# Kernel tuning notes

Measured on AMD Instinct MI355X. Metric: run time of the kernel, lower is better.

The kernel has to match this reference:

```python
import jax, jax.numpy as jnp
import numpy as np

T_LEN, E_LEN, BATCH, DIM = 32, 256, 16, 512  # topic_len, exp_len, batch, input=hidden size
HID = 512


def setup_inputs() -> dict:
    key = jax.random.key(0)
    k1, k2, k3, k4, k5, k6 = jax.random.split(key, 6)
    topic = jax.random.normal(k1, (T_LEN, BATCH, DIM), dtype=jnp.float32)
    exp_output = jax.random.normal(k2, (E_LEN, BATCH, DIM), dtype=jnp.float32)
    seq_mask = jax.random.bernoulli(k3, 0.1, (E_LEN, BATCH))  # True = masked exp position
    # nn.Linear(hidden+input, hidden): weight [HID, HID+DIM], bias [HID]
    lim1 = 1.0 / np.sqrt(HID + DIM)
    W_attn = jax.random.uniform(k4, (HID, HID + DIM), minval=-lim1, maxval=lim1, dtype=jnp.float32)
    b_attn = jax.random.uniform(k5, (HID,), minval=-lim1, maxval=lim1, dtype=jnp.float32)
    # nn.Linear(hidden, 1): weight [1, HID], bias [1]
    lim2 = 1.0 / np.sqrt(HID)
    kv, kb = jax.random.split(k6)
    v_score = jax.random.uniform(kv, (1, HID), minval=-lim2, maxval=lim2, dtype=jnp.float32)
    b_score = jax.random.uniform(kb, (1,), minval=-lim2, maxval=lim2, dtype=jnp.float32)
    return {"topic": topic, "exp_output": exp_output, "seq_mask": seq_mask,
            "W_attn": W_attn, "b_attn": b_attn, "v_score": v_score, "b_score": b_score}


def reference(topic, exp_output, seq_mask, W_attn, b_attn, v_score, b_score):
    # topic: [T, B, D]; exp_output: [E, B, D]; seq_mask: [E, B] bool
    D = topic.shape[2]
    # Split the concat-Linear: cat(topic, exp) @ W.T == topic @ W[:, :D].T + exp @ W[:, D:].T
    proj_t = jnp.einsum('tbd,hd->bth', topic, W_attn[:, :D])        # [B, T, H]
    proj_e = jnp.einsum('ebd,hd->beh', exp_output, W_attn[:, D:])   # [B, E, H]
    feat = jnp.tanh(proj_t[:, :, None, :] + proj_e[:, None, :, :] + b_attn)  # [B, T, E, H]
    energies = jnp.einsum('bteh,h->bte', feat, v_score[0]) + b_score[0]      # [B, T, E]
    # mask exp positions (broadcast over topic dim), as masked_fill(-1e12)
    energies = jnp.where(seq_mask.T[:, None, :], jnp.float32(-1e12), energies)
    attn_s1 = jax.nn.softmax(jnp.swapaxes(energies, 1, 2), axis=2)  # [B, E, T], softmax over topics
    attn_s2 = jax.nn.softmax(energies, axis=2)                      # [B, T, E], softmax over exp
    new_exp = jnp.einsum('bet,btd->bed', attn_s1, jnp.swapaxes(topic, 0, 1))       # [B, E, D]
    new_topic = jnp.einsum('bte,bed->btd', attn_s2, jnp.swapaxes(exp_output, 0, 1))  # [B, T, D]
    return new_topic, new_exp
```

## Files before the change

### kernel.cpp

```cpp
#include <hip/hip_runtime.h>
#include <hip/hip_bf16.h>
#include <cstddef>
#include <cstdint>

#define T_LEN 32
#define E_LEN 256
#define BATCH 16
#define DIM 512
#define HID 512
#define WROW 1024

#define TWO_LOG2E 2.8853900817779268f
#define LOG2E 1.4426950408889634f

typedef __attribute__((ext_vector_type(8))) short bf16x8;
typedef __attribute__((ext_vector_type(4))) float f32x4;

__device__ inline bf16x8 cvt8(float4 a, float4 b) {
    union { bf16x8 v; __hip_bfloat16 h[8]; } u;
    u.h[0] = __float2bfloat16(a.x); u.h[1] = __float2bfloat16(a.y);
    u.h[2] = __float2bfloat16(a.z); u.h[3] = __float2bfloat16(a.w);
    u.h[4] = __float2bfloat16(b.x); u.h[5] = __float2bfloat16(b.y);
    u.h[6] = __float2bfloat16(b.z); u.h[7] = __float2bfloat16(b.w);
    return u.v;
}

#define GPAD 8
#define GLDR (64 + GPAD)

__global__ __launch_bounds__(256) void gemm_fused(
    const float* __restrict__ topic, const float* __restrict__ expo,
    const float* __restrict__ W, const float* __restrict__ battn,
    float* __restrict__ EPT, float* __restrict__ EPE) {
    __shared__ __hip_bfloat16 As[64 * GLDR];
    __shared__ __hip_bfloat16 Bs[64 * GLDR];
    const int tid = threadIdx.x;
    const int by = blockIdx.y;
    const float* A; const float* Wp; const float* bias; float* C; int m0;
    if (by < 8) { A = topic; Wp = W;       bias = battn;   C = EPT; m0 = by * 64; }
    else        { A = expo;  Wp = W + DIM; bias = nullptr; C = EPE; m0 = (by - 8) * 64; }
    const int n0 = blockIdx.x * 64;
    const int w = tid >> 6;
    const int lane = tid & 63;
    const int l15 = lane & 15;
    const int g = lane >> 4;
    const int srow = tid >> 2;
    const int sc = tid & 3;

    f32x4 acc[4];
    const f32x4 z = {0.f, 0.f, 0.f, 0.f};
#pragma unroll
    for (int nt = 0; nt < 4; ++nt) acc[nt] = z;

    const float* ga = A + (size_t)(m0 + srow) * 512 + sc * 8;
    const float* gb = Wp + (size_t)(n0 + srow) * WROW + sc * 8;

    float4 a0 = *(const float4*)(ga);
    float4 a1 = *(const float4*)(ga + 4);
    float4 a2 = *(const float4*)(ga + 32);
    float4 a3 = *(const float4*)(ga + 36);
    float4 b0 = *(const float4*)(gb);
    float4 b1 = *(const float4*)(gb + 4);
    float4 b2 = *(const float4*)(gb + 32);
    float4 b3 = *(const float4*)(gb + 36);

    for (int kk = 0; kk < 8; ++kk) {
        bf16x8 av0 = cvt8(a0, a1), av1 = cvt8(a2, a3);
        bf16x8 bv0 = cvt8(b0, b1), bv1 = cvt8(b2, b3);
        if (kk < 7) {
            ga += 64; gb += 64;
            a0 = *(const float4*)(ga);
            a1 = *(const float4*)(ga + 4);
            a2 = *(const float4*)(ga + 32);
            a3 = *(const float4*)(ga + 36);
            b0 = *(const float4*)(gb);
            b1 = *(const float4*)(gb + 4);
            b2 = *(const float4*)(gb + 32);
            b3 = *(const float4*)(gb + 36);
        }
        __syncthreads();
        *(bf16x8*)&As[srow * GLDR + sc * 8] = av0;
        *(bf16x8*)&As[srow * GLDR + sc * 8 + 32] = av1;
        *(bf16x8*)&Bs[srow * GLDR + sc * 8] = bv0;
        *(bf16x8*)&Bs[srow * GLDR + sc * 8 + 32] = bv1;
        __syncthreads();
#pragma unroll
        for (int s = 0; s < 2; ++s) {
            bf16x8 af = *(const bf16x8*)&As[(w * 16 + l15) * GLDR + (s * 4 + g) * 8];
#pragma unroll
            for (int nt = 0; nt < 4; ++nt) {
                bf16x8 bf = *(const bf16x8*)&Bs[(nt * 16 + l15) * GLDR + (s * 4 + g) * 8];
                acc[nt] = __builtin_amdgcn_mfma_f32_16x16x32_bf16(af, bf, acc[nt], 0, 0, 0);
            }
        }
    }
#pragma unroll
    for (int nt = 0; nt < 4; ++nt) {
        int n = n0 + nt * 16 + l15;
        float bv = bias ? bias[n] : 0.f;
#pragma unroll
        for (int r = 0; r < 4; ++r) {
            int m = m0 + w * 16 + g * 4 + r;
            C[(size_t)m * 512 + n] = __builtin_amdgcn_exp2f((acc[nt][r] + bv) * TWO_LOG2E);
        }
    }
}

__global__ __launch_bounds__(256) void energies_k(const float* __restrict__ EPT,
                                                  const float* __restrict__ EPE,
                                                  const float* __restrict__ v,
                                                  const int* __restrict__ mask,
                                                  float* __restrict__ P) {
    const int b = blockIdx.x;
    const int tg = blockIdx.y;
    const int ech = blockIdx.z;
    const int lane = threadIdx.x & 63;
    const int w = threadIdx.x >> 6;
    const int h0 = lane * 8;
    const int e0 = ech * 16 + w * 4;

    int mk[4];
#pragma unroll
    for (int ei = 0; ei < 4; ++ei) mk[ei] = mask[(e0 + ei) * BATCH + b];

    float sv[8], spt[8][8];
    {
        float4 v0 = *(const float4*)(v + h0);
        float4 v1 = *(const float4*)(v + h0 + 4);
        sv[0] = -2.f * v0.x; sv[1] = -2.f * v0.y; sv[2] = -2.f * v0.z; sv[3] = -2.f * v0.w;
        sv[4] = -2.f * v1.x; sv[5] = -2.f * v1.y; sv[6] = -2.f * v1.z; sv[7] = -2.f * v1.w;
#pragma unroll
        for (int i = 0; i < 8; ++i) {
            const float* p = EPT + ((size_t)((tg * 8 + i) * BATCH + b)) * HID + h0;
            float4 p0 = *(const float4*)(p);
            float4 p1 = *(const float4*)(p + 4);
            spt[i][0] = p0.x; spt[i][1] = p0.y; spt[i][2] = p0.z; spt[i][3] = p0.w;
            spt[i][4] = p1.x; spt[i][5] = p1.y; spt[i][6] = p1.z; spt[i][7] = p1.w;
        }
    }
#pragma unroll
    for (int ei = 0; ei < 4; ++ei) {
        const int e = e0 + ei;
        if (mk[ei] != 0) {
            if (lane < 8)
                P[((size_t)b * T_LEN + tg * 8 + lane) * E_LEN + e] = 1e-30f;
            continue;
        }
        const float* pe = EPE + ((size_t)(e * BATCH + b)) * HID + h0;
        float4 p0 = *(const float4*)(pe);
        float4 p1 = *(const float4*)(pe + 4);
        float pr[8] = {p0.x, p0.y, p0.z, p0.w, p1.x, p1.y, p1.z, p1.w};
        float a[8] = {0.f, 0.f, 0.f, 0.f, 0.f, 0.f, 0.f, 0.f};
#pragma unroll
        for (int i = 0; i < 8; ++i) {
#pragma unroll
            for (int j = 0; j < 8; ++j) {
                float q = fmaf(spt[i][j], pr[j], 1.0f);
                float r = __builtin_amdgcn_rcpf(q);
                a[i] = fmaf(sv[j], r, a[i]);
            }
        }
#pragma unroll
        for (int i = 0; i < 8; ++i) {
            a[i] += __shfl_xor(a[i], 1);
            a[i] += __shfl_xor(a[i], 2);
            a[i] += __shfl_xor(a[i], 4);
            a[i] += __shfl_xor(a[i], 8);
        }
        const int sel = lane & 3;
        float uA = sel == 0 ? a[0] : sel == 1 ? a[1] : sel == 2 ? a[2] : a[3];
        float uB = sel == 0 ? a[4] : sel == 1 ? a[5] : sel == 2 ? a[6] : a[7];
        uA += __shfl_xor(uA, 16); uA += __shfl_xor(uA, 32);
        uB += __shfl_xor(uB, 16); uB += __shfl_xor(uB, 32);
        float u = (lane & 4) ? uB : uA;
        if (lane < 8)
            P[((size_t)b * T_LEN + tg * 8 + lane) * E_LEN + e] =
                __builtin_amdgcn_exp2f(u * LOG2E);
    }
}

__global__ __launch_bounds__(256) void epilogue_k(const float* __restrict__ P,
                                                  const float* __restrict__ topic,
                                                  const float* __restrict__ expo,
                                                  float* __restrict__ out) {
    __shared__ float smem[2560];
    const int tid = threadIdx.x;
    const int lane = tid & 63;
    const int w = tid >> 6;
    if (blockIdx.x < 512) {
        const int b = blockIdx.x >> 5;
        const int ech = (blockIdx.x >> 1) & 15;
        const int hf = blockIdx.x & 1;
        const int e0 = ech * 16 + w * 4;
        float wv[4];
#pragma unroll
        for (int ei = 0; ei < 4; ++ei) {
            const int e = e0 + ei;
            float x = (lane < T_LEN) ? P[((size_t)b * T_LEN + lane) * E_LEN + e] : 0.f;
            float s = x;
#pragma unroll
            for (int off = 32; off; off >>= 1) s += __shfl_xor(s, off);
            wv[ei] = x * __builtin_amdgcn_rcpf(s);
        }
        const int d0 = hf * 256 + lane * 4;
        float4 acc[4];
#pragma unroll
        for (int ei = 0; ei < 4; ++ei) acc[ei] = {0.f, 0.f, 0.f, 0.f};
        for (int t = 0; t < T_LEN; ++t) {
            float4 r = *(const float4*)(topic + ((size_t)t * BATCH + b) * DIM + d0);
            float wt[4];
#pragma unroll
            for (int ei = 0; ei < 4; ++ei) wt[ei] = __shfl(wv[ei], t);
#pragma unroll
            for (int ei = 0; ei < 4; ++ei) {
                acc[ei].x = fmaf(wt[ei], r.x, acc[ei].x);
                acc[ei].y = fmaf(wt[ei], r.y, acc[ei].y);
                acc[ei].z = fmaf(wt[ei], r.z, acc[ei].z);
                acc[ei].w = fmaf(wt[ei], r.w, acc[ei].w);
            }
        }
#pragma unroll
        for (int ei = 0; ei < 4; ++ei) {
            float* o = out + (size_t)BATCH * T_LEN * DIM +
                       ((size_t)b * E_LEN + e0 + ei) * DIM + d0;
            *(float4*)o = acc[ei];
        }
    } else {
        const int q = blockIdx.x - 512;
        const int b = q >> 5;
        const int tp = (q >> 1) & 15;
        const int hf = q & 1;
        if (w < 2) {
            const int bt = b * T_LEN + tp * 2 + w;
            float4 xv = *(const float4*)&P[(size_t)bt * E_LEN + lane * 4];
            float s = xv.x + xv.y + xv.z + xv.w;
#pragma unroll
            for (int off = 32; off; off >>= 1) s += __shfl_xor(s, off);
            float inv = __builtin_amdgcn_rcpf(s);
            float4 wvv = {xv.x * inv, xv.y * inv, xv.z * inv, xv.w * inv};
            *(float4*)&smem[w * 256 + lane * 4] = wvv;
        }
        __syncthreads();
        const int dl = lane * 4;
        const int dglob = hf * 256 + dl;
        float4 a0 = {0.f, 0.f, 0.f, 0.f};
        float4 a1 = {0.f, 0.f, 0.f, 0.f};
        const float* base = expo + (size_t)b * DIM + dglob;
        for (int ee = 0; ee < 64; ++ee) {
            const int e = w * 64 + ee;
            float4 rv = *(const float4*)(base + (size_t)e * BATCH * DIM);
            float w0 = smem[e];
            float w1 = smem[256 + e];
            a0.x = fmaf(w0, rv.x, a0.x); a0.y = fmaf(w0, rv.y, a0.y);
            a0.z = fmaf(w0, rv.z, a0.z); a0.w = fmaf(w0, rv.w, a0.w);
            a1.x = fmaf(w1, rv.x, a1.x); a1.y = fmaf(w1, rv.y, a1.y);
            a1.z = fmaf(w1, rv.z, a1.z); a1.w = fmaf(w1, rv.w, a1.w);
        }
        *(float4*)&smem[512 + (w * 2 + 0) * 256 + dl] = a0;
        *(float4*)&smem[512 + (w * 2 + 1) * 256 + dl] = a1;
        __syncthreads();
#pragma unroll
        for (int tt = 0; tt < 2; ++tt) {
            float sum = smem[512 + (0 * 2 + tt) * 256 + tid] +
                        smem[512 + (1 * 2 + tt) * 256 + tid] +
                        smem[512 + (2 * 2 + tt) * 256 + tid] +
                        smem[512 + (3 * 2 + tt) * 256 + tid];
            out[((size_t)b * T_LEN + tp * 2 + tt) * DIM + hf * 256 + tid] = sum;
        }
    }
}

extern "C" void kernel_launch(void* const* d_in, const int* in_sizes, int n_in,
                              void* d_out, int out_size, void* d_ws, size_t ws_size,
                              hipStream_t stream) {
    const float* topic = (const float*)d_in[0];
    const float* expo  = (const float*)d_in[1];
    const int*   mask  = (const int*)d_in[2];
    const float* W     = (const float*)d_in[3];
    const float* battn = (const float*)d_in[4];
    const float* vsc   = (const float*)d_in[5];
    float* out = (float*)d_out;

    float* EPT = (float*)d_ws;
    float* EPE = EPT + (size_t)T_LEN * BATCH * HID;
    float* P   = EPE + (size_t)E_LEN * BATCH * HID;

    gemm_fused<<<dim3(8, 72), 256, 0, stream>>>(topic, expo, W, battn, EPT, EPE);
    energies_k<<<dim3(BATCH, 4, 16), 256, 0, stream>>>(EPT, EPE, vsc, mask, P);
    epilogue_k<<<1024, 256, 0, stream>>>(P, topic, expo, out);
}
```

Before: 114.5 us.

## Store exp-side projection in bf16 and widen new_topic blocks to four topics

The GEMM now writes the exp(2*proj_e) intermediate as bf16 instead of fp32, and energies_k reads eight bf16 values per lane. This halves the traffic of the largest intermediate buffer at some cost in precision. The new_topic half of the epilogue now handles four topic rows per block instead of two, which halves how often the exp_output rows are reloaded and cuts that part of the grid from 512 to 256 blocks. All grids are flattened to 1D with the same index mapping.

```diff
diff --git a/kernel.cpp b/kernel.cpp
--- a/kernel.cpp
+++ b/kernel.cpp
@@ -28,18 +28,19 @@
 #define GPAD 8
 #define GLDR (64 + GPAD)
 
-__global__ __launch_bounds__(256) void gemm_fused(
+__global__ __launch_bounds__(256) void gemm_fused_k(
     const float* __restrict__ topic, const float* __restrict__ expo,
     const float* __restrict__ W, const float* __restrict__ battn,
-    float* __restrict__ EPT, float* __restrict__ EPE) {
+    float* __restrict__ EPT, __hip_bfloat16* __restrict__ EPE) {
     __shared__ __hip_bfloat16 As[64 * GLDR];
     __shared__ __hip_bfloat16 Bs[64 * GLDR];
     const int tid = threadIdx.x;
-    const int by = blockIdx.y;
-    const float* A; const float* Wp; const float* bias; float* C; int m0;
-    if (by < 8) { A = topic; Wp = W;       bias = battn;   C = EPT; m0 = by * 64; }
-    else        { A = expo;  Wp = W + DIM; bias = nullptr; C = EPE; m0 = (by - 8) * 64; }
-    const int n0 = blockIdx.x * 64;
+    const int by = blockIdx.x >> 3;
+    const int n0 = (blockIdx.x & 7) * 64;
+    const float* A; const float* Wp; int m0;
+    const bool isT = (by < 8);
+    if (isT) { A = topic; Wp = W;       m0 = by * 64; }
+    else     { A = expo;  Wp = W + DIM; m0 = (by - 8) * 64; }
     const int w = tid >> 6;
     const int lane = tid & 63;
     const int l15 = lane & 15;
@@ -94,28 +95,43 @@
             }
         }
     }
-#pragma unroll
-    for (int nt = 0; nt < 4; ++nt) {
-        int n = n0 + nt * 16 + l15;
-        float bv = bias ? bias[n] : 0.f;
-#pragma unroll
-        for (int r = 0; r < 4; ++r) {
-            int m = m0 + w * 16 + g * 4 + r;
-            C[(size_t)m * 512 + n] = __builtin_amdgcn_exp2f((acc[nt][r] + bv) * TWO_LOG2E);
-        }
-    }
-}
-
-__global__ __launch_bounds__(256) void energies_k(const float* __restrict__ EPT,
-                                                  const float* __restrict__ EPE,
-                                                  const float* __restrict__ v,
-                                                  const int* __restrict__ mask,
-                                                  float* __restrict__ P) {
-    const int b = blockIdx.x;
-    const int tg = blockIdx.y;
-    const int ech = blockIdx.z;
-    const int lane = threadIdx.x & 63;
-    const int w = threadIdx.x >> 6;
+    if (isT) {
+#pragma unroll
+        for (int nt = 0; nt < 4; ++nt) {
+            int n = n0 + nt * 16 + l15;
+            float bv = battn[n];
+#pragma unroll
+            for (int r = 0; r < 4; ++r) {
+                int m = m0 + w * 16 + g * 4 + r;
+                EPT[(size_t)m * 512 + n] =
+                    __builtin_amdgcn_exp2f((acc[nt][r] + bv) * TWO_LOG2E);
+            }
+        }
+    } else {
+#pragma unroll
+        for (int nt = 0; nt < 4; ++nt) {
+            int n = n0 + nt * 16 + l15;
+#pragma unroll
+            for (int r = 0; r < 4; ++r) {
+                int m = m0 + w * 16 + g * 4 + r;
+                EPE[(size_t)m * 512 + n] = __float2bfloat16(
+                    __builtin_amdgcn_exp2f(acc[nt][r] * TWO_LOG2E));
+            }
+        }
+    }
+}
+
+__global__ __launch_bounds__(256) void energies_k(
+    const float* __restrict__ EPT, const __hip_bfloat16* __restrict__ EPE,
+    const float* __restrict__ v, const int* __restrict__ mask,
+    float* __restrict__ P) {
+    const int u = blockIdx.x;
+    const int b = u & 15;
+    const int tg = (u >> 4) & 3;
+    const int ech = u >> 6;
+    const int tid = threadIdx.x;
+    const int lane = tid & 63;
+    const int w = tid >> 6;
     const int h0 = lane * 8;
     const int e0 = ech * 16 + w * 4;
 
@@ -146,10 +162,11 @@
                 P[((size_t)b * T_LEN + tg * 8 + lane) * E_LEN + e] = 1e-30f;
             continue;
         }
-        const float* pe = EPE + ((size_t)(e * BATCH + b)) * HID + h0;
-        float4 p0 = *(const float4*)(pe);
-        float4 p1 = *(const float4*)(pe + 4);
-        float pr[8] = {p0.x, p0.y, p0.z, p0.w, p1.x, p1.y, p1.z, p1.w};
+        union { bf16x8 v8; __hip_bfloat16 h[8]; } pv;
+        pv.v8 = *(const bf16x8*)(EPE + ((size_t)(e * BATCH + b)) * HID + h0);
+        float pr[8];
+#pragma unroll
+        for (int j = 0; j < 8; ++j) pr[j] = __bfloat162float(pv.h[j]);
         float a[8] = {0.f, 0.f, 0.f, 0.f, 0.f, 0.f, 0.f, 0.f};
 #pragma unroll
         for (int i = 0; i < 8; ++i) {
@@ -172,18 +189,17 @@
         float uB = sel == 0 ? a[4] : sel == 1 ? a[5] : sel == 2 ? a[6] : a[7];
         uA += __shfl_xor(uA, 16); uA += __shfl_xor(uA, 32);
         uB += __shfl_xor(uB, 16); uB += __shfl_xor(uB, 32);
-        float u = (lane & 4) ? uB : uA;
+        float uu = (lane & 4) ? uB : uA;
         if (lane < 8)
             P[((size_t)b * T_LEN + tg * 8 + lane) * E_LEN + e] =
-                __builtin_amdgcn_exp2f(u * LOG2E);
-    }
-}
-
-__global__ __launch_bounds__(256) void epilogue_k(const float* __restrict__ P,
-                                                  const float* __restrict__ topic,
-                                                  const float* __restrict__ expo,
-                                                  float* __restrict__ out) {
-    __shared__ float smem[2560];
+                __builtin_amdgcn_exp2f(uu * LOG2E);
+    }
+}
+
+__global__ __launch_bounds__(256) void epilogue_k(
+    const float* __restrict__ P, const float* __restrict__ topic,
+    const float* __restrict__ expo, float* __restrict__ out) {
+    __shared__ float smem[5120];
     const int tid = threadIdx.x;
     const int lane = tid & 63;
     const int w = tid >> 6;
@@ -227,11 +243,11 @@
         }
     } else {
         const int q = blockIdx.x - 512;
-        const int b = q >> 5;
-        const int tp = (q >> 1) & 15;
+        const int b = q >> 4;
+        const int tq = (q >> 1) & 7;
         const int hf = q & 1;
-        if (w < 2) {
-            const int bt = b * T_LEN + tp * 2 + w;
+        {
+            const int bt = b * T_LEN + tq * 4 + w;
             float4 xv = *(const float4*)&P[(size_t)bt * E_LEN + lane * 4];
             float s = xv.x + xv.y + xv.z + xv.w;
 #pragma unroll
@@ -245,27 +261,37 @@
         const int dglob = hf * 256 + dl;
         float4 a0 = {0.f, 0.f, 0.f, 0.f};
         float4 a1 = {0.f, 0.f, 0.f, 0.f};
+        float4 a2 = {0.f, 0.f, 0.f, 0.f};
+        float4 a3 = {0.f, 0.f, 0.f, 0.f};
         const float* base = expo + (size_t)b * DIM + dglob;
         for (int ee = 0; ee < 64; ++ee) {
             const int e = w * 64 + ee;
             float4 rv = *(const float4*)(base + (size_t)e * BATCH * DIM);
             float w0 = smem[e];
             float w1 = smem[256 + e];
+            float w2 = smem[512 + e];
+            float w3 = smem[768 + e];
             a0.x = fmaf(w0, rv.x, a0.x); a0.y = fmaf(w0, rv.y, a0.y);
             a0.z = fmaf(w0, rv.z, a0.z); a0.w = fmaf(w0, rv.w, a0.w);
             a1.x = fmaf(w1, rv.x, a1.x); a1.y = fmaf(w1, rv.y, a1.y);
             a1.z = fmaf(w1, rv.z, a1.z); a1.w = fmaf(w1, rv.w, a1.w);
-        }
-        *(float4*)&smem[512 + (w * 2 + 0) * 256 + dl] = a0;
-        *(float4*)&smem[512 + (w * 2 + 1) * 256 + dl] = a1;
+            a2.x = fmaf(w2, rv.x, a2.x); a2.y = fmaf(w2, rv.y, a2.y);
+            a2.z = fmaf(w2, rv.z, a2.z); a2.w = fmaf(w2, rv.w, a2.w);
+            a3.x = fmaf(w3, rv.x, a3.x); a3.y = fmaf(w3, rv.y, a3.y);
+            a3.z = fmaf(w3, rv.z, a3.z); a3.w = fmaf(w3, rv.w, a3.w);
+        }
+        *(float4*)&smem[1024 + (w * 4 + 0) * 256 + dl] = a0;
+        *(float4*)&smem[1024 + (w * 4 + 1) * 256 + dl] = a1;
+        *(float4*)&smem[1024 + (w * 4 + 2) * 256 + dl] = a2;
+        *(float4*)&smem[1024 + (w * 4 + 3) * 256 + dl] = a3;
         __syncthreads();
 #pragma unroll
-        for (int tt = 0; tt < 2; ++tt) {
-            float sum = smem[512 + (0 * 2 + tt) * 256 + tid] +
-                        smem[512 + (1 * 2 + tt) * 256 + tid] +
-                        smem[512 + (2 * 2 + tt) * 256 + tid] +
-                        smem[512 + (3 * 2 + tt) * 256 + tid];
-            out[((size_t)b * T_LEN + tp * 2 + tt) * DIM + hf * 256 + tid] = sum;
+        for (int tt = 0; tt < 4; ++tt) {
+            float sum = smem[1024 + (0 * 4 + tt) * 256 + tid] +
+                        smem[1024 + (1 * 4 + tt) * 256 + tid] +
+                        smem[1024 + (2 * 4 + tt) * 256 + tid] +
+                        smem[1024 + (3 * 4 + tt) * 256 + tid];
+            out[((size_t)b * T_LEN + tq * 4 + tt) * DIM + hf * 256 + tid] = sum;
         }
     }
 }
@@ -282,10 +308,10 @@
     float* out = (float*)d_out;
 
     float* EPT = (float*)d_ws;
-    float* EPE = EPT + (size_t)T_LEN * BATCH * HID;
-    float* P   = EPE + (size_t)E_LEN * BATCH * HID;
-
-    gemm_fused<<<dim3(8, 72), 256, 0, stream>>>(topic, expo, W, battn, EPT, EPE);
-    energies_k<<<dim3(BATCH, 4, 16), 256, 0, stream>>>(EPT, EPE, vsc, mask, P);
-    epilogue_k<<<1024, 256, 0, stream>>>(P, topic, expo, out);
-}
+    __hip_bfloat16* EPE = (__hip_bfloat16*)(EPT + 512 * 512);
+    float* P = (float*)(EPE + (size_t)4096 * 512);
+
+    gemm_fused_k<<<576, 256, 0, stream>>>(topic, expo, W, battn, EPT, EPE);
+    energies_k<<<1024, 256, 0, stream>>>(EPT, EPE, vsc, mask, P);
+    epilogue_k<<<768, 256, 0, stream>>>(P, topic, expo, out);
+}
```

Measured after the change: 113.9 us. Within noise of the previous version (-0.6%).
